# Kernel tuning notes

Measured on AMD Instinct MI355X. Metric: run time of the kernel, lower is better.

The kernel has to match this reference:

```python
import jax, jax.numpy as jnp
import numpy as np

NUM_HEADS = 6
KS = 3  # kernel_size


def _offset_vectors():
    # torch: arange(-s//2+1, s//2+1) with s=3 -> [-1, 0, 1]; meshgrid 'ij'; stack last; reshape(27,3)
    r = jnp.arange(-(KS // 2), KS // 2 + 1, dtype=jnp.float32)
    gi, gj, gt = jnp.meshgrid(r, r, r, indexing='ij')
    return jnp.stack([gi, gj, gt], -1).reshape(KS ** 3, 3)  # [27, 3]


def setup_inputs() -> dict:
    key = jax.random.key(0)
    kq, kk, kr = jax.random.split(key, 3)
    B, H, W, T, C = 1, 64, 64, 64, 96
    q = jax.random.normal(kq, (B, H, W, T, C), dtype=jnp.float32)
    k = jax.random.normal(kk, (B, H, W, T, C), dtype=jnp.float32)
    rpb = jax.random.normal(kr, (NUM_HEADS, KS, KS, KS), dtype=jnp.float32) * 0.02
    return {"q": q, "k": k, "rpb": rpb}


def reference(q, k, rpb):
    B, H, W, T, C = q.shape
    nh, hd = NUM_HEADS, C // NUM_HEADS
    scale = hd ** (-0.5)
    pdr = (KS - 1) // 2

    qh = q.reshape(B, H, W, T, nh, hd) * scale           # [B,H,W,T,nh,hd]
    kh = k.reshape(B, H, W, T, nh, hd)
    kp = jnp.pad(kh, ((0, 0), (pdr, pdr), (pdr, pdr), (pdr, pdr), (0, 0), (0, 0)))

    # Neighborhood attention logits: dot(q, k_neighbor) + rpb  -> [B,H,W,T,nh,KS^3]
    logits = []
    for di in range(KS):
        for dj in range(KS):
            for dt in range(KS):
                kw = kp[:, di:di + H, dj:dj + W, dt:dt + T]   # shifted window
                a = jnp.einsum('bhwtnc,bhwtnc->bhwtn', qh, kw) + rpb[:, di, dj, dt]
                logits.append(a)
    attn = jnp.stack(logits, -1)                         # [B,H,W,T,nh,27]
    attn = jax.nn.softmax(attn, axis=-1)

    v = _offset_vectors()                                 # [27, 3]
    x = attn @ v                                          # [B,H,W,T,nh,3]
    # -> [B, nh, 3, H, W, T] -> [B, nh*3, H, W, T]
    x = jnp.transpose(x, (0, 4, 5, 1, 2, 3)).reshape(B, nh * 3, H, W, T)
    return x
```

## Files before the change

kernel.cpp:

```cpp
#include <hip/hip_runtime.h>


#define DH 64
#define DW 64
#define DT 64
#define DC 96
#define NH 6
#define HD 16

__device__ __forceinline__ float quad_reduce_add(float x) {
    int i = __float_as_int(x);
    i = __builtin_amdgcn_mov_dpp(i, 0xB1, 0xF, 0xF, true);
    x += __int_as_float(i);
    i = __float_as_int(x);
    i = __builtin_amdgcn_mov_dpp(i, 0x4E, 0xF, 0xF, true);
    x += __int_as_float(i);
    return x;
}

__global__ __launch_bounds__(384) void natten3d_kernel(
    const float* __restrict__ q,
    const float* __restrict__ k,
    const float* __restrict__ rpb,
    float* __restrict__ out)
{
    int bid = blockIdx.x;
    int nb  = (bid & 7) * 2048 + (bid >> 3);
    int tile = nb & 3;
    int w    = (nb >> 2) & 63;
    int h    = nb >> 8;

    int tid  = threadIdx.x;
    int s    = tid & 3;
    int r    = tid >> 2;
    int n    = r % NH;
    int tloc = r / NH;
    int t    = tile * 16 + tloc;

    const float* qp = q + ((size_t)((h * DW + w) * DT + t)) * DC + n * HD + s * 4;
    float4 q4 = *reinterpret_cast<const float4*>(qp);
    q4.x *= 0.25f; q4.y *= 0.25f; q4.z *= 0.25f; q4.w *= 0.25f;

    int  coff[9];
    bool cok[9];
    #pragma unroll
    for (int c = 0; c < 9; ++c) {
        int di = c / 3, dj = c % 3;
        int hh = h + di - 1, ww = w + dj - 1;
        cok[c] = ((unsigned)hh < DH) && ((unsigned)ww < DW);
        int hc = min(max(hh, 0), DH - 1);
        int wc = min(max(ww, 0), DW - 1);
        coff[c] = (hc * DW + wc) * DT * DC;
    }

    int  voff[3];
    bool dok[3];
    #pragma unroll
    for (int d = 0; d < 3; ++d) {
        int tt = t + d - 1;
        dok[d] = (unsigned)tt < DT;
        int ttc = min(max(tt, 0), DT - 1);
        voff[d] = ttc * DC + n * HD + s * 4;
    }

    float l = 0.f, a0 = 0.f, a1 = 0.f, a2 = 0.f;
    const int rbase = n * 27;

    #pragma unroll
    for (int g = 0; g < 3; ++g) {
        float4 kb[9];
        float  rb[9];
        #pragma unroll
        for (int j = 0; j < 9; ++j) {
            const int c = g * 3 + j / 3;
            const int d = j % 3;
            kb[j] = *reinterpret_cast<const float4*>(k + (size_t)(coff[c] + voff[d]));
            rb[j] = rpb[rbase + g * 9 + j];
        }
        #pragma unroll
        for (int j = 0; j < 9; ++j) {
            const int c = g * 3 + j / 3;
            const int d = j % 3;
            float part = q4.x * kb[j].x;
            part = fmaf(q4.y, kb[j].y, part);
            part = fmaf(q4.z, kb[j].z, part);
            part = fmaf(q4.w, kb[j].w, part);
            part = (cok[c] && dok[d]) ? part : 0.f;
            float dot = quad_reduce_add(part);
            float p = __expf(dot + rb[j]);
            l += p;
            if (g == 0)      a0 -= p; else if (g == 2)      a0 += p;
            if (j / 3 == 0)  a1 -= p; else if (j / 3 == 2)  a1 += p;
            if (d == 0)      a2 -= p; else if (d == 2)      a2 += p;
        }
    }

    float inv = 1.f / l;
    float res = ((s == 0) ? a0 : (s == 1) ? a1 : a2) * inv;
    size_t plane = (size_t)DH * DW * DT;
    size_t sp = (size_t)(h * DW + w) * DT + t;
    if (s < 3) out[(size_t)(n * 3 + s) * plane + sp] = res;
}

extern "C" void kernel_launch(void* const* d_in, const int* in_sizes, int n_in,
                              void* d_out, int out_size, void* d_ws, size_t ws_size,
                              hipStream_t stream) {
    const float* q   = (const float*)d_in[0];
    const float* k   = (const float*)d_in[1];
    const float* rpb = (const float*)d_in[2];
    float* out = (float*)d_out;

    dim3 grid(DH * DW * 4);
    dim3 block(16 * NH * 4);
    hipLaunchKernelGGL(natten3d_kernel, grid, block, 0, stream, q, k, rpb, out);
}
```

Before: 323.0 us.

## Process four time steps per quad to reuse sliding-window key loads

Each quad of threads now handles four consecutive time positions instead of one. Per spatial neighbor it loads six key vectors shared across the overlapping temporal windows, rather than three per output. After the quad reduction, each lane keeps only its own time step's dot products, so the exp and softmax work is spread across the quad and every lane writes all three outputs. The change cuts redundant key loads and makes the grid four times smaller, at the cost of more registers for q and keys and four times more dot-product FMAs and DPP reductions per thread.

New measurement: 271.3 us. 1.19x faster.

```diff
diff --git a/kernel.cpp b/kernel.cpp
--- a/kernel.cpp
+++ b/kernel.cpp
@@ -25,21 +25,27 @@
     float* __restrict__ out)
 {
     int bid = blockIdx.x;
-    int nb  = (bid & 7) * 2048 + (bid >> 3);
-    int tile = nb & 3;
-    int w    = (nb >> 2) & 63;
-    int h    = nb >> 8;
+    int nb  = (bid & 7) * 512 + (bid >> 3);
+    int h = nb >> 6;
+    int w = nb & 63;
 
     int tid  = threadIdx.x;
     int s    = tid & 3;
     int r    = tid >> 2;
     int n    = r % NH;
-    int tloc = r / NH;
-    int t    = tile * 16 + tloc;
+    int t0   = (r / NH) * 4;
+    int tout = t0 + s;
 
-    const float* qp = q + ((size_t)((h * DW + w) * DT + t)) * DC + n * HD + s * 4;
-    float4 q4 = *reinterpret_cast<const float4*>(qp);
-    q4.x *= 0.25f; q4.y *= 0.25f; q4.z *= 0.25f; q4.w *= 0.25f;
+    float4 qv[4];
+    {
+        const float* qp = q + ((size_t)((h * DW + w) * DT + t0)) * DC + n * HD + s * 4;
+        #pragma unroll
+        for (int u = 0; u < 4; ++u) {
+            float4 v = *reinterpret_cast<const float4*>(qp + u * DC);
+            v.x *= 0.25f; v.y *= 0.25f; v.z *= 0.25f; v.w *= 0.25f;
+            qv[u] = v;
+        }
+    }
 
     int  coff[9];
     bool cok[9];
@@ -53,53 +59,66 @@
         coff[c] = (hc * DW + wc) * DT * DC;
     }
 
-    int  voff[3];
-    bool dok[3];
+    int soff[6];
     #pragma unroll
-    for (int d = 0; d < 3; ++d) {
-        int tt = t + d - 1;
-        dok[d] = (unsigned)tt < DT;
-        int ttc = min(max(tt, 0), DT - 1);
-        voff[d] = ttc * DC + n * HD + s * 4;
+    for (int j = 0; j < 6; ++j) {
+        int tt = min(max(t0 + j - 1, 0), DT - 1);
+        soff[j] = tt * DC + n * HD + s * 4;
     }
 
-    float l = 0.f, a0 = 0.f, a1 = 0.f, a2 = 0.f;
+    float acc_l = 0.f, acc0 = 0.f, acc1 = 0.f, acc2 = 0.f;
     const int rbase = n * 27;
 
     #pragma unroll
-    for (int g = 0; g < 3; ++g) {
-        float4 kb[9];
-        float  rb[9];
+    for (int c = 0; c < 9; ++c) {
+        const int di = c / 3, dj = c % 3;
+
+        float4 kb[6];
         #pragma unroll
-        for (int j = 0; j < 9; ++j) {
-            const int c = g * 3 + j / 3;
-            const int d = j % 3;
-            kb[j] = *reinterpret_cast<const float4*>(k + (size_t)(coff[c] + voff[d]));
-            rb[j] = rpb[rbase + g * 9 + j];
+        for (int j = 0; j < 6; ++j)
+            kb[j] = *reinterpret_cast<const float4*>(k + (size_t)(coff[c] + soff[j]));
+
+        float rb0 = rpb[rbase + c * 3 + 0];
+        float rb1 = rpb[rbase + c * 3 + 1];
+        float rb2 = rpb[rbase + c * 3 + 2];
+
+        float kd0 = 0.f, kd1 = 0.f, kd2 = 0.f;
+        #pragma unroll
+        for (int u = 0; u < 4; ++u) {
+            #pragma unroll
+            for (int d = 0; d < 3; ++d) {
+                const int j = u + d;
+                float p = qv[u].x * kb[j].x;
+                p = fmaf(qv[u].y, kb[j].y, p);
+                p = fmaf(qv[u].z, kb[j].z, p);
+                p = fmaf(qv[u].w, kb[j].w, p);
+                float dot = quad_reduce_add(p);
+                const bool mine = (s == u);
+                if (d == 0)      kd0 = mine ? dot : kd0;
+                else if (d == 1) kd1 = mine ? dot : kd1;
+                else             kd2 = mine ? dot : kd2;
+            }
         }
+
         #pragma unroll
-        for (int j = 0; j < 9; ++j) {
-            const int c = g * 3 + j / 3;
-            const int d = j % 3;
-            float part = q4.x * kb[j].x;
-            part = fmaf(q4.y, kb[j].y, part);
-            part = fmaf(q4.z, kb[j].z, part);
-            part = fmaf(q4.w, kb[j].w, part);
-            part = (cok[c] && dok[d]) ? part : 0.f;
-            float dot = quad_reduce_add(part);
-            float p = __expf(dot + rb[j]);
-            l += p;
-            if (g == 0)      a0 -= p; else if (g == 2)      a0 += p;
-            if (j / 3 == 0)  a1 -= p; else if (j / 3 == 2)  a1 += p;
-            if (d == 0)      a2 -= p; else if (d == 2)      a2 += p;
+        for (int d = 0; d < 3; ++d) {
+            float dot = (d == 0) ? kd0 : (d == 1) ? kd1 : kd2;
+            bool valid = cok[c] && ((unsigned)(tout + d - 1) < DT);
+            float logit = (valid ? dot : 0.f) + ((d == 0) ? rb0 : (d == 1) ? rb1 : rb2);
+            float p = __expf(logit);
+            acc_l += p;
+            if (di == 0) acc0 -= p; else if (di == 2) acc0 += p;
+            if (dj == 0) acc1 -= p; else if (dj == 2) acc1 += p;
+            if (d  == 0) acc2 -= p; else if (d  == 2) acc2 += p;
         }
     }
 
-    float inv = 1.f / l;
-    float res = ((s == 0) ? a0 : (s == 1) ? a1 : a2) * inv;
+    float inv = 1.f / acc_l;
     size_t plane = (size_t)DH * DW * DT;
-    size_t sp = (size_t)(h * DW + w) * DT + t;
-    if (s < 3) out[(size_t)(n * 3 + s) * plane + sp] = res;
+    size_t sp = (size_t)((h * DW + w) * DT) + tout;
+    out[(size_t)(n * 3 + 0) * plane + sp] = acc0 * inv;
+    out[(size_t)(n * 3 + 1) * plane + sp] = acc1 * inv;
+    out[(size_t)(n * 3 + 2) * plane + sp] = acc2 * inv;
 }
 
 extern "C" void kernel_launch(void* const* d_in, const int* in_sizes, int n_in,
@@ -110,7 +129,7 @@
     const float* rpb = (const float*)d_in[2];
     float* out = (float*)d_out;
 
-    dim3 grid(DH * DW * 4);
+    dim3 grid(DH * DW);
     dim3 block(16 * NH * 4);
     hipLaunchKernelGGL(natten3d_kernel, grid, block, 0, stream, q, k, rpb, out);
 }
```
